# Kernel optimization log

Measured on AMD Instinct MI355X. Metric: run time of the kernel, lower is better.

The kernel has to match this reference:

```python
import jax, jax.numpy as jnp
import numpy as np

D = 2048
N_HEADS = 16
N_KV = 4
HEAD_DIM = D // N_HEADS  # 128
N_REP = N_HEADS // N_KV  # 4
B, S = 2, 2048


def setup_inputs() -> dict:
    key = jax.random.key(0)
    ks = jax.random.split(key, 5)
    scale = 0.02
    return {
        "x": jax.random.normal(ks[0], (B, S, D), dtype=jnp.float32),
        "wq": jax.random.normal(ks[1], (D, N_HEADS * HEAD_DIM), dtype=jnp.float32) * scale,
        "wk": jax.random.normal(ks[2], (D, N_KV * HEAD_DIM), dtype=jnp.float32) * scale,
        "wv": jax.random.normal(ks[3], (D, N_KV * HEAD_DIM), dtype=jnp.float32) * scale,
        "wo": jax.random.normal(ks[4], (N_HEADS * HEAD_DIM, D), dtype=jnp.float32) * scale,
    }


def reference(x, wq, wk, wv, wo):
    b, s, _ = x.shape
    # projections
    xq = (x @ wq).reshape(b, s, N_HEADS, HEAD_DIM)
    xk = (x @ wk).reshape(b, s, N_KV, HEAD_DIM)
    xv = (x @ wv).reshape(b, s, N_KV, HEAD_DIM)
    # GQA: group queries per kv head -> [b, n_kv, n_rep, s, d]
    xq = xq.transpose(0, 2, 1, 3).reshape(b, N_KV, N_REP, s, HEAD_DIM)
    xk = xk.transpose(0, 2, 1, 3)  # [b, n_kv, s, d]
    xv = xv.transpose(0, 2, 1, 3)
    scale = 1.0 / jnp.sqrt(jnp.asarray(HEAD_DIM, dtype=x.dtype))
    scores = jnp.einsum('bkrqd,bkvd->bkrqv', xq, xk) * scale  # [b,n_kv,n_rep,s,s]
    causal = jnp.triu(jnp.ones((s, s), dtype=bool), k=1)
    scores = jnp.where(causal, jnp.asarray(-jnp.inf, dtype=scores.dtype), scores)
    probs = jax.nn.softmax(scores, axis=-1)
    out = jnp.einsum('bkrqv,bkvd->bkrqd', probs, xv)  # [b,n_kv,n_rep,s,d]
    out = out.reshape(b, N_HEADS, s, HEAD_DIM).transpose(0, 2, 1, 3).reshape(b, s, N_HEADS * HEAD_DIM)
    return out @ wo
```

## Files before the change

kernel.cpp:

```cpp
#include <hip/hip_runtime.h>

typedef unsigned short u16;
using bf16x8 = __attribute__((ext_vector_type(8))) short;
using f32x4  = __attribute__((ext_vector_type(4))) float;

#define ATTN_NEG (-3.0e38f)

__device__ __forceinline__ u16 f2bf_rne(float f) {
  unsigned int u = __float_as_uint(f);
  u += 0x7fffu + ((u >> 16) & 1u);
  return (u16)(u >> 16);
}

__device__ __forceinline__ void load_lds16(const u16* g, u16* l) {
  using gp = const __attribute__((address_space(1))) unsigned int*;
  using lp = __attribute__((address_space(3))) unsigned int*;
  __builtin_amdgcn_global_load_lds((gp)g, (lp)l, 16, 0, 0);
}

__device__ __forceinline__ void transpose_body(const float* __restrict__ in,
                                               u16* __restrict__ out, int K, int N,
                                               int bx, int by, int tid) {
  __shared__ float tile[32][33];
  int tx = tid & 31, ty = tid >> 5;
  int x0 = bx * 32, y0 = by * 32;
  #pragma unroll
  for (int i = 0; i < 32; i += 8)
    tile[ty + i][tx] = in[(size_t)(y0 + ty + i) * N + x0 + tx];
  __syncthreads();
  #pragma unroll
  for (int i = 0; i < 32; i += 8)
    out[(size_t)(x0 + ty + i) * K + y0 + tx] = f2bf_rne(tile[tx][ty + i]);
}

__global__ __launch_bounds__(256) void prep_kernel(const float* __restrict__ x,
                                                   const float* __restrict__ wq,
                                                   const float* __restrict__ wk,
                                                   const float* __restrict__ wv,
                                                   const float* __restrict__ wo,
                                                   u16* xb, u16* wqt, u16* wkt, u16* wvt,
                                                   u16* wot) {
  int bid = blockIdx.x, tid = threadIdx.x;
  if (bid < 8192) {
    int i = bid * 1024 + tid * 4;
    float4 v = *(const float4*)(x + i);
    u16* p = xb + i;
    p[0] = f2bf_rne(v.x); p[1] = f2bf_rne(v.y); p[2] = f2bf_rne(v.z); p[3] = f2bf_rne(v.w);
  } else if (bid < 12288) {
    int t = bid - 8192;
    transpose_body(wq, wqt, 2048, 2048, t & 63, t >> 6, tid);
  } else if (bid < 13312) {
    int t = bid - 12288;
    transpose_body(wk, wkt, 2048, 512, t & 15, t >> 4, tid);
  } else if (bid < 14336) {
    int t = bid - 13312;
    transpose_body(wv, wvt, 2048, 512, t & 15, t >> 4, tid);
  } else {
    int t = bid - 14336;
    transpose_body(wo, wot, 2048, 2048, t & 63, t >> 6, tid);
  }
}

template <int MODE>
__device__ __forceinline__ void gemm_tile(const u16* __restrict__ A, const u16* __restrict__ Bt,
                                          void* __restrict__ Cv, int M, int N, int K,
                                          int bx, int by, char* smem) {
  u16* As = (u16*)smem;
  u16* Bs = (u16*)(smem + 16384);
  const int tid  = threadIdx.x;
  const int wave = tid >> 6, lane = tid & 63;
  const int quad = lane >> 4, l16 = lane & 15;
  const int m0 = by * 128, n0 = bx * 128;
  const int wm = (wave >> 1) * 64, wn = (wave & 1) * 64;
  f32x4 acc[4][4] = {};

  const int srow = lane >> 2;
  const int scol = (lane & 3) << 3;

  for (int k0 = 0; k0 < K; k0 += 64) {
    __syncthreads();
    #pragma unroll
    for (int h = 0; h < 2; ++h)
      #pragma unroll
      for (int i = 0; i < 2; ++i) {
        const int row = wave * 16 + i * 64;
        load_lds16(A  + (size_t)(m0 + row + srow) * K + k0 + h * 32 + scol,
                   As + h * 4096 + row * 32);
        load_lds16(Bt + (size_t)(n0 + row + srow) * K + k0 + h * 32 + scol,
                   Bs + h * 4096 + row * 32);
      }
    __syncthreads();
    #pragma unroll
    for (int h = 0; h < 2; ++h) {
      bf16x8 af[4], bfr[4];
      #pragma unroll
      for (int i = 0; i < 4; ++i) {
        af[i]  = *(const bf16x8*)(As + h * 4096 + (wm + i * 16 + l16) * 32 + quad * 8);
        bfr[i] = *(const bf16x8*)(Bs + h * 4096 + (wn + i * 16 + l16) * 32 + quad * 8);
      }
      #pragma unroll
      for (int mi = 0; mi < 4; ++mi)
        #pragma unroll
        for (int ni = 0; ni < 4; ++ni)
          acc[mi][ni] =
              __builtin_amdgcn_mfma_f32_16x16x32_bf16(af[mi], bfr[ni], acc[mi][ni], 0, 0, 0);
    }
  }

  if constexpr (MODE == 0 || MODE == 3) {
    const float sc = (MODE == 3) ? 0.12751742f : 1.0f;
    u16* Cb = (u16*)Cv;
    #pragma unroll
    for (int mi = 0; mi < 4; ++mi)
      #pragma unroll
      for (int ni = 0; ni < 4; ++ni) {
        int row = m0 + wm + mi * 16 + quad * 4;
        int col = n0 + wn + ni * 16 + l16;
        #pragma unroll
        for (int r = 0; r < 4; ++r)
          Cb[(size_t)(row + r) * N + col] = f2bf_rne(acc[mi][ni][r] * sc);
      }
  } else if constexpr (MODE == 1) {
    u16* Cb = (u16*)Cv;
    #pragma unroll
    for (int mi = 0; mi < 4; ++mi)
      #pragma unroll
      for (int ni = 0; ni < 4; ++ni) {
        int col = n0 + wn + ni * 16 + l16;
        #pragma unroll
        for (int r = 0; r < 4; ++r) {
          int row = m0 + wm + mi * 16 + quad * 4 + r;
          int bb = row >> 11, s = row & 2047;
          int c = s & 31;
          int cp = ((c & 15) >> 2) * 8 + ((c >> 4) & 1) * 4 + (c & 3);
          Cb[((size_t)(bb * 512 + col)) * 2048 + (s & ~31) + cp] = f2bf_rne(acc[mi][ni][r]);
        }
      }
  } else {
    float* Cf = (float*)Cv;
    #pragma unroll
    for (int mi = 0; mi < 4; ++mi)
      #pragma unroll
      for (int ni = 0; ni < 4; ++ni) {
        int row = m0 + wm + mi * 16 + quad * 4;
        int col = n0 + wn + ni * 16 + l16;
        #pragma unroll
        for (int r = 0; r < 4; ++r)
          Cf[(size_t)(row + r) * N + col] = acc[mi][ni][r];
      }
  }
}

__global__ __launch_bounds__(256) void qkv_gemm(const u16* xb, const u16* wqt, const u16* wkt,
                                                const u16* wvt, u16* Qb, u16* Kb, u16* Vt) {
  extern __shared__ char smem[];
  int bx = blockIdx.x, by = blockIdx.y;
  if (bx < 16)
    gemm_tile<3>(xb, wqt, Qb, 4096, 2048, 2048, bx, by, smem);
  else if (bx < 20)
    gemm_tile<0>(xb, wkt, Kb, 4096, 512, 2048, bx - 16, by, smem);
  else
    gemm_tile<1>(xb, wvt, Vt, 4096, 512, 2048, bx - 20, by, smem);
}

template <int MODE>
__global__ __launch_bounds__(256) void gemm_kernel(const u16* A, const u16* Bt, void* C,
                                                   int M, int N, int K) {
  extern __shared__ char smem[];
  gemm_tile<MODE>(A, Bt, C, M, N, K, blockIdx.x, blockIdx.y, smem);
}


__device__ __forceinline__ void stage_kv(const u16* __restrict__ Kg, const u16* __restrict__ Vg,
                                         int kt0, u16* __restrict__ kbuf, u16* __restrict__ vbuf,
                                         int wave, int quad, int l16) {
  #pragma unroll
  for (int h = 0; h < 2; ++h)
    load_lds16(Kg + (size_t)(kt0 + h * 16 + l16) * 512 + wave * 32 + quad * 8,
               kbuf + (wave * 2 + h) * 512);
  #pragma unroll
  for (int i = 0; i < 2; ++i) {
    int f = wave * 2 + i;
    load_lds16(Vg + (size_t)(16 * f + l16) * 2048 + kt0 + quad * 8, vbuf + f * 512);
  }
}

template <bool MASKED>
__device__ __forceinline__ void attn_compute(const u16* __restrict__ kbuf,
                                             const u16* __restrict__ vbuf,
                                             int kt0, int q0w, int quad, int l16,
                                             const bf16x8 (&qf)[4], f32x4 (&o)[8],
                                             float& l_lane) {
  const int slot = (quad * 16 + l16) * 8;
  bf16x8 kf[8];
  #pragma unroll
  for (int kk = 0; kk < 8; ++kk) kf[kk] = *(const bf16x8*)(kbuf + kk * 512 + slot);

  f32x4 sa[2] = {};
  __builtin_amdgcn_s_setprio(1);
  #pragma unroll
  for (int h = 0; h < 2; ++h)
    #pragma unroll
    for (int ks = 0; ks < 4; ++ks)
      sa[h] = __builtin_amdgcn_mfma_f32_16x16x32_bf16(kf[ks * 2 + h], qf[ks], sa[h], 0, 0, 0);
  __builtin_amdgcn_s_setprio(0);

  bf16x8 pc;
  #pragma unroll
  for (int h = 0; h < 2; ++h)
    #pragma unroll
    for (int r = 0; r < 4; ++r) {
      float s = sa[h][r];
      if (MASKED) {
        int kpos = kt0 + 16 * h + quad * 4 + r;
        s = (kpos <= q0w + l16) ? s : ATTN_NEG;
      }
      float p = __builtin_amdgcn_exp2f(s);
      l_lane += p;
      pc[h * 4 + r] = (short)f2bf_rne(p);
    }

  __builtin_amdgcn_s_setprio(1);
  #pragma unroll
  for (int f = 0; f < 8; ++f) {
    bf16x8 v8 = *(const bf16x8*)(vbuf + f * 512 + slot);
    o[f] = __builtin_amdgcn_mfma_f32_16x16x32_bf16(pc, v8, o[f], 0, 0, 0);
  }
  __builtin_amdgcn_s_setprio(0);
}

__global__ __launch_bounds__(256, 2) void attn_kernel(const u16* __restrict__ Qb,
                                                      const u16* __restrict__ Kb,
                                                      const u16* __restrict__ Vt,
                                                      u16* __restrict__ Ob) {
  constexpr int S = 2048;
  const int b = blockIdx.z, h = blockIdx.y, g = h >> 2, tp = blockIdx.x;
  const int tid = threadIdx.x;
  const int wave = tid >> 6, lane = tid & 63, quad = lane >> 4, l16 = lane & 15;
  __shared__ alignas(16) u16 Kt[3][4096];
  __shared__ alignas(16) u16 Vl[3][4096];
  __shared__ float lbuf[4][16];

  const u16* Kg = Kb + (size_t)b * S * 512 + g * 128;
  const u16* Vg = Vt + (size_t)(b * 512 + g * 128) * 2048;

  for (int half = 0; half < 2; ++half) {
    const int tile = (half == 0) ? tp : 31 - tp;
    const int wrow = (half == 0) ? wave : 3 - wave;
    const int q0w = tile * 64 + wrow * 16;
    const int nsteps = 2 * tile + 2;
    const int s_diag = 2 * tile + (wrow >> 1);

    bf16x8 qf[4];
    const u16* qrow = Qb + (size_t)(b * S + q0w + l16) * 2048 + h * 128 + quad * 8;
    #pragma unroll
    for (int ks = 0; ks < 4; ++ks) qf[ks] = *(const bf16x8*)(qrow + ks * 32);
    asm volatile("s_waitcnt vmcnt(0)" ::: "memory");
    #pragma unroll
    for (int ks = 0; ks < 4; ++ks)
      asm volatile("" : "+v"(qf[ks]));

    f32x4 o[8] = {};
    float l_lane = 0.f;

    __syncthreads();
    stage_kv(Kg, Vg, 0, Kt[0], Vl[0], wave, quad, l16);
    stage_kv(Kg, Vg, 32, Kt[1], Vl[1], wave, quad, l16);

    for (int s = 0; s < nsteps; ++s) {
      asm volatile("s_waitcnt vmcnt(4)" ::: "memory");
      __builtin_amdgcn_s_barrier();
      {
        const int sn = (s + 2 < nsteps) ? s + 2 : nsteps - 1;
        const int bn = (s + 2) % 3;
        stage_kv(Kg, Vg, sn * 32, Kt[bn], Vl[bn], wave, quad, l16);
      }
      const int bc = s % 3;
      if (s < s_diag)
        attn_compute<false>(Kt[bc], Vl[bc], s * 32, q0w, quad, l16, qf, o, l_lane);
      else if (s == s_diag)
        attn_compute<true>(Kt[bc], Vl[bc], s * 32, q0w, quad, l16, qf, o, l_lane);
    }
    asm volatile("s_waitcnt vmcnt(0)" ::: "memory");

    float lt = l_lane + __shfl_xor(l_lane, 16);
    lt += __shfl_xor(lt, 32);
    if (quad == 0) lbuf[wave][l16] = lt;
    __builtin_amdgcn_wave_barrier();
    float il[4];
    #pragma unroll
    for (int r = 0; r < 4; ++r) il[r] = 1.f / lbuf[wave][quad * 4 + r];

    u16* orow = Ob + (size_t)(b * S + q0w + quad * 4) * 2048 + h * 128 + l16;
    #pragma unroll
    for (int f = 0; f < 8; ++f)
      #pragma unroll
      for (int r = 0; r < 4; ++r)
        orow[(size_t)r * 2048 + f * 16] = f2bf_rne(o[f][r] * il[r]);
  }
}

extern "C" void kernel_launch(void* const* d_in, const int* in_sizes, int n_in,
                              void* d_out, int out_size, void* d_ws, size_t ws_size,
                              hipStream_t stream) {
  const float* x  = (const float*)d_in[0];
  const float* wq = (const float*)d_in[1];
  const float* wk = (const float*)d_in[2];
  const float* wv = (const float*)d_in[3];
  const float* wo = (const float*)d_in[4];
  float* out = (float*)d_out;
  char* ws = (char*)d_ws;

  u16* xb  = (u16*)(ws);
  u16* wqt = (u16*)(ws + 16777216);
  u16* wkt = (u16*)(ws + 25165824);
  u16* wvt = (u16*)(ws + 27262976);
  u16* wot = (u16*)(ws + 29360128);
  u16* Qb  = (u16*)(ws + 37748736);
  u16* Kb  = (u16*)(ws + 54525952);
  u16* Vt  = (u16*)(ws + 58720256);
  u16* Ab  = (u16*)(ws + 62914560);

  prep_kernel<<<18432, 256, 0, stream>>>(x, wq, wk, wv, wo, xb, wqt, wkt, wvt, wot);
  qkv_gemm<<<dim3(24, 32), 256, 32768, stream>>>(xb, wqt, wkt, wvt, Qb, Kb, Vt);
  attn_kernel<<<dim3(16, 16, 2), 256, 0, stream>>>(Qb, Kb, Vt, Ab);
  gemm_kernel<2><<<dim3(16, 32), 256, 32768, stream>>>(Ab, wot, out, 4096, 2048, 2048);
}
```

Baseline: 306.7 us.

## Split paired causal tiles into separate blocks with balanced ordering and double buffering

Stops having each attention block process a light and a heavy query tile in turn. The kernel now launches one block per query tile (1024 blocks) with a 1D index that interleaves short and long tiles for load balance. It shrinks the KV staging from triple to double buffering with a syncthreads each step, and raises launch bounds to 4 blocks per CU for more occupancy. The cost is a shallower prefetch pipeline and more per-block setup overhead.

After: 309.5 us. No clear change (+0.9%).

```diff
diff --git a/kernel.cpp b/kernel.cpp
--- a/kernel.cpp
+++ b/kernel.cpp
@@ -229,75 +229,63 @@
   __builtin_amdgcn_s_setprio(0);
 }
 
-__global__ __launch_bounds__(256, 2) void attn_kernel(const u16* __restrict__ Qb,
+__global__ __launch_bounds__(256, 4) void attn_kernel(const u16* __restrict__ Qb,
                                                       const u16* __restrict__ Kb,
                                                       const u16* __restrict__ Vt,
                                                       u16* __restrict__ Ob) {
   constexpr int S = 2048;
-  const int b = blockIdx.z, h = blockIdx.y, g = h >> 2, tp = blockIdx.x;
+  const int x = blockIdx.x;
+  const int k4 = x >> 8, r256 = x & 255;
+  const int j = r256 >> 5, bh = r256 & 31;
+  const int b = bh >> 4, h = bh & 15, g = h >> 2;
+  const int tile = (k4 == 0) ? j : (k4 == 1) ? (15 - j) : (k4 == 2) ? (16 + j) : (31 - j);
   const int tid = threadIdx.x;
   const int wave = tid >> 6, lane = tid & 63, quad = lane >> 4, l16 = lane & 15;
-  __shared__ alignas(16) u16 Kt[3][4096];
-  __shared__ alignas(16) u16 Vl[3][4096];
+  __shared__ alignas(16) u16 Kt[2][4096];
+  __shared__ alignas(16) u16 Vl[2][4096];
   __shared__ float lbuf[4][16];
 
   const u16* Kg = Kb + (size_t)b * S * 512 + g * 128;
   const u16* Vg = Vt + (size_t)(b * 512 + g * 128) * 2048;
 
-  for (int half = 0; half < 2; ++half) {
-    const int tile = (half == 0) ? tp : 31 - tp;
-    const int wrow = (half == 0) ? wave : 3 - wave;
-    const int q0w = tile * 64 + wrow * 16;
-    const int nsteps = 2 * tile + 2;
-    const int s_diag = 2 * tile + (wrow >> 1);
-
-    bf16x8 qf[4];
-    const u16* qrow = Qb + (size_t)(b * S + q0w + l16) * 2048 + h * 128 + quad * 8;
-    #pragma unroll
-    for (int ks = 0; ks < 4; ++ks) qf[ks] = *(const bf16x8*)(qrow + ks * 32);
-    asm volatile("s_waitcnt vmcnt(0)" ::: "memory");
-    #pragma unroll
-    for (int ks = 0; ks < 4; ++ks)
-      asm volatile("" : "+v"(qf[ks]));
-
-    f32x4 o[8] = {};
-    float l_lane = 0.f;
-
+  const int q0w = tile * 64 + wave * 16;
+  const int nsteps = 2 * tile + 2;
+  const int s_diag = 2 * tile + (wave >> 1);
+
+  bf16x8 qf[4];
+  const u16* qrow = Qb + (size_t)(b * S + q0w + l16) * 2048 + h * 128 + quad * 8;
+  #pragma unroll
+  for (int ks = 0; ks < 4; ++ks) qf[ks] = *(const bf16x8*)(qrow + ks * 32);
+
+  f32x4 o[8] = {};
+  float l_lane = 0.f;
+
+  stage_kv(Kg, Vg, 0, Kt[0], Vl[0], wave, quad, l16);
+
+  for (int s = 0; s < nsteps; ++s) {
     __syncthreads();
-    stage_kv(Kg, Vg, 0, Kt[0], Vl[0], wave, quad, l16);
-    stage_kv(Kg, Vg, 32, Kt[1], Vl[1], wave, quad, l16);
-
-    for (int s = 0; s < nsteps; ++s) {
-      asm volatile("s_waitcnt vmcnt(4)" ::: "memory");
-      __builtin_amdgcn_s_barrier();
-      {
-        const int sn = (s + 2 < nsteps) ? s + 2 : nsteps - 1;
-        const int bn = (s + 2) % 3;
-        stage_kv(Kg, Vg, sn * 32, Kt[bn], Vl[bn], wave, quad, l16);
-      }
-      const int bc = s % 3;
-      if (s < s_diag)
-        attn_compute<false>(Kt[bc], Vl[bc], s * 32, q0w, quad, l16, qf, o, l_lane);
-      else if (s == s_diag)
-        attn_compute<true>(Kt[bc], Vl[bc], s * 32, q0w, quad, l16, qf, o, l_lane);
-    }
-    asm volatile("s_waitcnt vmcnt(0)" ::: "memory");
-
-    float lt = l_lane + __shfl_xor(l_lane, 16);
-    lt += __shfl_xor(lt, 32);
-    if (quad == 0) lbuf[wave][l16] = lt;
-    __builtin_amdgcn_wave_barrier();
-    float il[4];
-    #pragma unroll
-    for (int r = 0; r < 4; ++r) il[r] = 1.f / lbuf[wave][quad * 4 + r];
-
-    u16* orow = Ob + (size_t)(b * S + q0w + quad * 4) * 2048 + h * 128 + l16;
-    #pragma unroll
-    for (int f = 0; f < 8; ++f)
-      #pragma unroll
-      for (int r = 0; r < 4; ++r)
-        orow[(size_t)r * 2048 + f * 16] = f2bf_rne(o[f][r] * il[r]);
-  }
+    if (s + 1 < nsteps)
+      stage_kv(Kg, Vg, (s + 1) * 32, Kt[(s + 1) & 1], Vl[(s + 1) & 1], wave, quad, l16);
+    if (s < s_diag)
+      attn_compute<false>(Kt[s & 1], Vl[s & 1], s * 32, q0w, quad, l16, qf, o, l_lane);
+    else if (s == s_diag)
+      attn_compute<true>(Kt[s & 1], Vl[s & 1], s * 32, q0w, quad, l16, qf, o, l_lane);
+  }
+
+  float lt = l_lane + __shfl_xor(l_lane, 16);
+  lt += __shfl_xor(lt, 32);
+  if (quad == 0) lbuf[wave][l16] = lt;
+  __builtin_amdgcn_wave_barrier();
+  float il[4];
+  #pragma unroll
+  for (int rr = 0; rr < 4; ++rr) il[rr] = 1.f / lbuf[wave][quad * 4 + rr];
+
+  u16* orow = Ob + (size_t)(b * S + q0w + quad * 4) * 2048 + h * 128 + l16;
+  #pragma unroll
+  for (int f = 0; f < 8; ++f)
+    #pragma unroll
+    for (int rr = 0; rr < 4; ++rr)
+      orow[(size_t)rr * 2048 + f * 16] = f2bf_rne(o[f][rr] * il[rr]);
 }
 
 extern "C" void kernel_launch(void* const* d_in, const int* in_sizes, int n_in,
@@ -323,6 +311,6 @@
 
   prep_kernel<<<18432, 256, 0, stream>>>(x, wq, wk, wv, wo, xb, wqt, wkt, wvt, wot);
   qkv_gemm<<<dim3(24, 32), 256, 32768, stream>>>(xb, wqt, wkt, wvt, Qb, Kb, Vt);
-  attn_kernel<<<dim3(16, 16, 2), 256, 0, stream>>>(Qb, Kb, Vt, Ab);
+  attn_kernel<<<1024, 256, 0, stream>>>(Qb, Kb, Vt, Ab);
   gemm_kernel<2><<<dim3(16, 32), 256, 32768, stream>>>(Ab, wot, out, 4096, 2048, 2048);
 }
```

## Switch attention KV pipeline to double-buffered 64-key stages

Applied to the files above, without the earlier changes.

The attention loop now stages 64 keys per step in two LDS buffers instead of 32 keys across three buffers. This halves the number of steps and block-wide barriers. The causal diagonal is handled in the last step, and a per-wave early break skips the fully masked 32-key chunk. The hand-written vmcnt waits and Q register pinning are removed, so the code relies on __syncthreads for memory ordering. The trade-off is shallower prefetch, more LDS per block, and a full memory wait at each barrier, which may expose load latency.

New measurement: 304.1 us. Within noise of the previous version (-0.9%).

```diff
diff --git a/kernel.cpp b/kernel.cpp
--- a/kernel.cpp
+++ b/kernel.cpp
@@ -171,62 +171,74 @@
 }
 
 
-__device__ __forceinline__ void stage_kv(const u16* __restrict__ Kg, const u16* __restrict__ Vg,
-                                         int kt0, u16* __restrict__ kbuf, u16* __restrict__ vbuf,
-                                         int wave, int quad, int l16) {
-  #pragma unroll
-  for (int h = 0; h < 2; ++h)
-    load_lds16(Kg + (size_t)(kt0 + h * 16 + l16) * 512 + wave * 32 + quad * 8,
-               kbuf + (wave * 2 + h) * 512);
-  #pragma unroll
-  for (int i = 0; i < 2; ++i) {
-    int f = wave * 2 + i;
-    load_lds16(Vg + (size_t)(16 * f + l16) * 2048 + kt0 + quad * 8, vbuf + f * 512);
+__device__ __forceinline__ void stage_kv64(const u16* __restrict__ Kg, const u16* __restrict__ Vg,
+                                           int kt0, u16* __restrict__ kbuf,
+                                           u16* __restrict__ vbuf,
+                                           int wave, int quad, int l16) {
+  #pragma unroll
+  for (int c = 0; c < 2; ++c) {
+    #pragma unroll
+    for (int h = 0; h < 2; ++h)
+      load_lds16(Kg + (size_t)(kt0 + 32 * c + h * 16 + l16) * 512 + wave * 32 + quad * 8,
+                 kbuf + c * 4096 + (wave * 2 + h) * 512);
+    #pragma unroll
+    for (int i = 0; i < 2; ++i) {
+      int f = wave * 2 + i;
+      load_lds16(Vg + (size_t)(16 * f + l16) * 2048 + kt0 + 32 * c + quad * 8,
+                 vbuf + c * 4096 + f * 512);
+    }
   }
 }
 
 template <bool MASKED>
-__device__ __forceinline__ void attn_compute(const u16* __restrict__ kbuf,
-                                             const u16* __restrict__ vbuf,
-                                             int kt0, int q0w, int quad, int l16,
-                                             const bf16x8 (&qf)[4], f32x4 (&o)[8],
-                                             float& l_lane) {
+__device__ __forceinline__ void attn_compute64(const u16* __restrict__ kbuf,
+                                               const u16* __restrict__ vbuf,
+                                               int kt0, int q0w, int quad, int l16,
+                                               const bf16x8 (&qf)[4], f32x4 (&o)[8],
+                                               float& l_lane) {
   const int slot = (quad * 16 + l16) * 8;
-  bf16x8 kf[8];
-  #pragma unroll
-  for (int kk = 0; kk < 8; ++kk) kf[kk] = *(const bf16x8*)(kbuf + kk * 512 + slot);
-
-  f32x4 sa[2] = {};
-  __builtin_amdgcn_s_setprio(1);
-  #pragma unroll
-  for (int h = 0; h < 2; ++h)
-    #pragma unroll
-    for (int ks = 0; ks < 4; ++ks)
-      sa[h] = __builtin_amdgcn_mfma_f32_16x16x32_bf16(kf[ks * 2 + h], qf[ks], sa[h], 0, 0, 0);
-  __builtin_amdgcn_s_setprio(0);
-
-  bf16x8 pc;
-  #pragma unroll
-  for (int h = 0; h < 2; ++h)
-    #pragma unroll
-    for (int r = 0; r < 4; ++r) {
-      float s = sa[h][r];
-      if (MASKED) {
-        int kpos = kt0 + 16 * h + quad * 4 + r;
-        s = (kpos <= q0w + l16) ? s : ATTN_NEG;
-      }
-      float p = __builtin_amdgcn_exp2f(s);
-      l_lane += p;
-      pc[h * 4 + r] = (short)f2bf_rne(p);
+  #pragma unroll
+  for (int c = 0; c < 2; ++c) {
+    const int kb = kt0 + 32 * c;
+    if (MASKED && kb > q0w + 15) break;
+
+    bf16x8 kf[8];
+    #pragma unroll
+    for (int kk = 0; kk < 8; ++kk)
+      kf[kk] = *(const bf16x8*)(kbuf + c * 4096 + kk * 512 + slot);
+
+    f32x4 sa[2] = {};
+    __builtin_amdgcn_s_setprio(1);
+    #pragma unroll
+    for (int h = 0; h < 2; ++h)
+      #pragma unroll
+      for (int ks = 0; ks < 4; ++ks)
+        sa[h] = __builtin_amdgcn_mfma_f32_16x16x32_bf16(kf[ks * 2 + h], qf[ks], sa[h], 0, 0, 0);
+    __builtin_amdgcn_s_setprio(0);
+
+    bf16x8 pc;
+    #pragma unroll
+    for (int h = 0; h < 2; ++h)
+      #pragma unroll
+      for (int r = 0; r < 4; ++r) {
+        float s = sa[h][r];
+        if (MASKED) {
+          int kpos = kb + 16 * h + quad * 4 + r;
+          s = (kpos <= q0w + l16) ? s : ATTN_NEG;
+        }
+        float p = __builtin_amdgcn_exp2f(s);
+        l_lane += p;
+        pc[h * 4 + r] = (short)f2bf_rne(p);
+      }
+
+    __builtin_amdgcn_s_setprio(1);
+    #pragma unroll
+    for (int f = 0; f < 8; ++f) {
+      bf16x8 v8 = *(const bf16x8*)(vbuf + c * 4096 + f * 512 + slot);
+      o[f] = __builtin_amdgcn_mfma_f32_16x16x32_bf16(pc, v8, o[f], 0, 0, 0);
     }
-
-  __builtin_amdgcn_s_setprio(1);
-  #pragma unroll
-  for (int f = 0; f < 8; ++f) {
-    bf16x8 v8 = *(const bf16x8*)(vbuf + f * 512 + slot);
-    o[f] = __builtin_amdgcn_mfma_f32_16x16x32_bf16(pc, v8, o[f], 0, 0, 0);
-  }
-  __builtin_amdgcn_s_setprio(0);
+    __builtin_amdgcn_s_setprio(0);
+  }
 }
 
 __global__ __launch_bounds__(256, 2) void attn_kernel(const u16* __restrict__ Qb,
@@ -237,51 +249,40 @@
   const int b = blockIdx.z, h = blockIdx.y, g = h >> 2, tp = blockIdx.x;
   const int tid = threadIdx.x;
   const int wave = tid >> 6, lane = tid & 63, quad = lane >> 4, l16 = lane & 15;
-  __shared__ alignas(16) u16 Kt[3][4096];
-  __shared__ alignas(16) u16 Vl[3][4096];
+  __shared__ alignas(16) u16 Kt[2][8192];
+  __shared__ alignas(16) u16 Vl[2][8192];
   __shared__ float lbuf[4][16];
 
   const u16* Kg = Kb + (size_t)b * S * 512 + g * 128;
   const u16* Vg = Vt + (size_t)(b * 512 + g * 128) * 2048;
 
+  #pragma unroll
   for (int half = 0; half < 2; ++half) {
     const int tile = (half == 0) ? tp : 31 - tp;
     const int wrow = (half == 0) ? wave : 3 - wave;
     const int q0w = tile * 64 + wrow * 16;
-    const int nsteps = 2 * tile + 2;
-    const int s_diag = 2 * tile + (wrow >> 1);
+    const int nsteps = tile + 1;
 
     bf16x8 qf[4];
     const u16* qrow = Qb + (size_t)(b * S + q0w + l16) * 2048 + h * 128 + quad * 8;
     #pragma unroll
     for (int ks = 0; ks < 4; ++ks) qf[ks] = *(const bf16x8*)(qrow + ks * 32);
-    asm volatile("s_waitcnt vmcnt(0)" ::: "memory");
-    #pragma unroll
-    for (int ks = 0; ks < 4; ++ks)
-      asm volatile("" : "+v"(qf[ks]));
 
     f32x4 o[8] = {};
     float l_lane = 0.f;
 
     __syncthreads();
-    stage_kv(Kg, Vg, 0, Kt[0], Vl[0], wave, quad, l16);
-    stage_kv(Kg, Vg, 32, Kt[1], Vl[1], wave, quad, l16);
+    stage_kv64(Kg, Vg, 0, Kt[0], Vl[0], wave, quad, l16);
 
     for (int s = 0; s < nsteps; ++s) {
-      asm volatile("s_waitcnt vmcnt(4)" ::: "memory");
-      __builtin_amdgcn_s_barrier();
-      {
-        const int sn = (s + 2 < nsteps) ? s + 2 : nsteps - 1;
-        const int bn = (s + 2) % 3;
-        stage_kv(Kg, Vg, sn * 32, Kt[bn], Vl[bn], wave, quad, l16);
-      }
-      const int bc = s % 3;
-      if (s < s_diag)
-        attn_compute<false>(Kt[bc], Vl[bc], s * 32, q0w, quad, l16, qf, o, l_lane);
-      else if (s == s_diag)
-        attn_compute<true>(Kt[bc], Vl[bc], s * 32, q0w, quad, l16, qf, o, l_lane);
+      __syncthreads();
+      if (s + 1 < nsteps)
+        stage_kv64(Kg, Vg, (s + 1) * 64, Kt[(s + 1) & 1], Vl[(s + 1) & 1], wave, quad, l16);
+      if (s + 1 < nsteps)
+        attn_compute64<false>(Kt[s & 1], Vl[s & 1], s * 64, q0w, quad, l16, qf, o, l_lane);
+      else
+        attn_compute64<true>(Kt[s & 1], Vl[s & 1], s * 64, q0w, quad, l16, qf, o, l_lane);
     }
-    asm volatile("s_waitcnt vmcnt(0)" ::: "memory");
 
     float lt = l_lane + __shfl_xor(l_lane, 16);
     lt += __shfl_xor(lt, 32);
```
